# Kernel optimization log

Measured on AMD Instinct MI355X. Metric: run time of the kernel, lower is better.

Reference implementation:

```python
import jax, jax.numpy as jnp
import numpy as np

N = 16384      # tokens
D_IN = 256     # input feature dim
D = 1024       # d_model
H = 2048       # expert hidden dim (2 * d_model)
E = 8          # n_experts
K = 2          # top_k
OUT = 2        # output classes
EPS = 1e-5


def layernorm(x, g, b):
    m = jnp.mean(x, axis=-1, keepdims=True)
    v = jnp.mean(jnp.square(x - m), axis=-1, keepdims=True)
    return (x - m) * jax.lax.rsqrt(v + EPS) * g + b


def setup_inputs() -> dict:
    key = jax.random.key(0)
    ks = jax.random.split(key, 10)
    s_in = 1.0 / np.sqrt(D_IN)
    s_d = 1.0 / np.sqrt(D)
    s_h = 1.0 / np.sqrt(H)
    return {
        "x": jax.random.normal(ks[0], (N, D_IN), jnp.float32),
        "w_in": jax.random.normal(ks[1], (D_IN, D), jnp.float32) * s_in,
        "b_in": jnp.zeros((D,), jnp.float32),
        "g_in": jnp.ones((D,), jnp.float32),
        "beta_in": jnp.zeros((D,), jnp.float32),
        "w_gate": jax.random.normal(ks[2], (D, E), jnp.float32) * s_d,
        "w1": jax.random.normal(ks[3], (E, D, H), jnp.float32) * s_d,
        "b1": jnp.zeros((E, H), jnp.float32),
        "w2": jax.random.normal(ks[4], (E, H, D), jnp.float32) * s_h,
        "b2": jnp.zeros((E, D), jnp.float32),
        "g_moe": jnp.ones((D,), jnp.float32),
        "beta_moe": jnp.zeros((D,), jnp.float32),
        "g_out": jnp.ones((D,), jnp.float32),
        "beta_out": jnp.zeros((D,), jnp.float32),
        "w_cls": jax.random.normal(ks[5], (D, OUT), jnp.float32) * s_d,
        "b_cls": jnp.zeros((OUT,), jnp.float32),
    }


def reference(x, w_in, b_in, g_in, beta_in, w_gate, w1, b1, w2, b2,
              g_moe, beta_moe, g_out, beta_out, w_cls, b_cls):
    # input projection + norm
    h = layernorm(x @ w_in + b_in, g_in, beta_in)            # [N, D]
    # router: softmax then top-k, renormalize over selected experts
    probs = jax.nn.softmax(h @ w_gate, axis=-1)              # [N, E]
    _, top_idx = jax.lax.top_k(probs, K)                     # [N, K]
    sel = jax.nn.one_hot(top_idx, E, dtype=probs.dtype).sum(axis=1)  # [N, E] 0/1
    gates = probs * sel
    gates = gates / (jnp.sum(gates, axis=-1, keepdims=True) + 1e-9)
    # experts: weighted combine; gate==0 tokens contribute nothing (same math
    # as the torch masked gather/scatter-add, dropout off in eval)
    mixed = jnp.zeros_like(h)
    for e in range(E):  # fixed, small expert count
        expert_out = jax.nn.gelu(h @ w1[e] + b1[e]) @ w2[e] + b2[e]  # [N, D]
        mixed = mixed + gates[:, e:e + 1] * expert_out
    out = layernorm(h + mixed, g_moe, beta_moe)
    out = layernorm(out, g_out, beta_out)
    return out @ w_cls + b_cls                               # [N, OUT]
```

## Files before the change

kernel.cpp:

```cpp
#include <hip/hip_runtime.h>
#include <hip/hip_bf16.h>

#define D_IN 256
#define DM   1024
#define HD   2048
#define NE   8
#define NTOK 16384

typedef __attribute__((ext_vector_type(8))) short short8;
typedef __attribute__((ext_vector_type(4))) float f32x4;
typedef unsigned int uint;

#define MT_TOFF1 0
#define MT_TOFF2 512
#define MT_CNT1  1536
#define MT_P1    1600
#define MT_OFF1  1664
#define MT_CNT2  1728
#define MT_PCNT2 1856
#define MT_TOTAL 1984

__device__ inline ushort f2bf(float v){
  __hip_bfloat16 b = __float2bfloat16(v);
  return *reinterpret_cast<ushort*>(&b);
}
__device__ inline float bf2f(ushort u){
  __hip_bfloat16 b = *reinterpret_cast<__hip_bfloat16*>(&u);
  return __bfloat162float(b);
}

__device__ inline float gelu_fast(float x){
  float u = 0.7978845608028654f * x * (1.0f + 0.044715f*x*x);
  return x / (1.0f + __expf(-2.0f*u));
}

__device__ inline void gload16(const void* g, void* l){
  __builtin_amdgcn_global_load_lds(
      (const __attribute__((address_space(1))) void*)g,
      (__attribute__((address_space(3))) void*)l, 16, 0, 0);
}

__global__ __launch_bounds__(256) void transpose_bf16_kernel(
    const float* __restrict__ src, ushort* __restrict__ dst, int R, int C)
{
  __shared__ float tile[32][33];
  int e = blockIdx.z;
  src += (size_t)e*R*C; dst += (size_t)e*R*C;
  int c0 = blockIdx.x*32, r0 = blockIdx.y*32;
  int tx = threadIdx.x & 31, ty = threadIdx.x >> 5;
  #pragma unroll
  for (int rr = ty; rr < 32; rr += 8)
    tile[rr][tx] = src[(size_t)(r0+rr)*C + c0+tx];
  __syncthreads();
  #pragma unroll
  for (int rr = ty; rr < 32; rr += 8)
    dst[(size_t)(c0+rr)*R + r0+tx] = f2bf(tile[tx][rr]);
}

__global__ __launch_bounds__(64) void build_xs6(
    const float* __restrict__ x, ushort* __restrict__ xs6)
{
  int row = blockIdx.x; int t = threadIdx.x;
  const float* xr = x + (size_t)row*D_IN;
  ushort* o = xs6 + (size_t)row*1536;
  #pragma unroll
  for (int i=0;i<4;++i){
    int c = t*4+i;
    float f = xr[c];
    ushort h = f2bf(f);        float fh = bf2f(h);
    ushort m = f2bf(f - fh);   float fm = bf2f(m);
    ushort lo = f2bf(f - fh - fm);
    o[c]      = h;  o[512+c]  = h;  o[1280+c] = h;
    o[256+c]  = m;  o[768+c]  = m;
    o[1024+c] = lo;
  }
}

__global__ __launch_bounds__(256) void build_wt6(
    const float* __restrict__ src, ushort* __restrict__ dst)
{
  __shared__ float tile[32][33];
  int c0 = blockIdx.x*32, r0 = blockIdx.y*32;
  int tx = threadIdx.x & 31, ty = threadIdx.x >> 5;
  #pragma unroll
  for (int rr = ty; rr < 32; rr += 8)
    tile[rr][tx] = src[(size_t)(r0+rr)*DM + c0+tx];
  __syncthreads();
  #pragma unroll
  for (int rr = ty; rr < 32; rr += 8){
    float f = tile[tx][rr];
    ushort h = f2bf(f);        float fh = bf2f(h);
    ushort m = f2bf(f - fh);   float fm = bf2f(m);
    ushort lo = f2bf(f - fh - fm);
    ushort* d = dst + (size_t)(c0+rr)*1536 + r0 + tx;
    d[0]    = h;  d[256]  = h;  d[1024] = h;
    d[512]  = m;  d[768]  = m;
    d[1280] = lo;
  }
}

__global__ __launch_bounds__(256) void wgate_t_kernel(
    const float* __restrict__ w_gate, float* __restrict__ wgt)
{
  int e = blockIdx.x;
  for (int j = threadIdx.x; j < DM; j += 256)
    wgt[(size_t)e*DM + j] = w_gate[(size_t)j*NE + e];
}

template<int MODE>
__global__ __launch_bounds__(512, 2) void gemm8p(
    const ushort* __restrict__ A,
    const ushort* __restrict__ BT,
    const int*   __restrict__ rows,
    const uint*  __restrict__ pcnt,
    const uint*  __restrict__ off1,
    const float* __restrict__ bias,
    float* __restrict__ yout,
    ushort* __restrict__ t1,
    int N, int K, int CH)
{
  __shared__ ushort lds[2][2][2][8192];
  const int tid = threadIdx.x;
  const int wid = tid>>6, l = tid&63;
  const int wm = wid>>2, wn = wid&3;
  const int lr = l&15, lk = l>>4;

  int e = 0;
  const int bn0 = blockIdx.x*256;
  const int bm0 = blockIdx.y*256;
  if (MODE==1){
    e = blockIdx.z;
    if ((uint)bm0 >= pcnt[e]) return;
  }
  const ushort* Bbase = BT + (MODE==1 ? (size_t)e*N*K : (size_t)0);

  const ushort* aS[2][2]; const ushort* bS[2][2];
  #pragma unroll
  for (int h=0;h<2;++h){
    #pragma unroll
    for (int j=0;j<2;++j){
      int idx = j*512 + tid;
      int r   = idx>>3;
      int cb  = ((idx&7)*16) ^ (((r>>2)&1)<<5);
      if (MODE==1){
        int id = rows[e*CH + bm0 + h*128 + r];
        aS[h][j] = A + (size_t)id*K + (cb>>1);
      } else {
        aS[h][j] = A + (size_t)(bm0 + h*128 + r)*K + (cb>>1);
      }
      bS[h][j] = Bbase + (size_t)(bn0 + h*128 + r)*K + (cb>>1);
    }
  }

  auto stageA = [&](int db, int kt){
    #pragma unroll
    for (int h=0;h<2;++h)
      #pragma unroll
      for (int j=0;j<2;++j)
        gload16(aS[h][j] + kt, &lds[db][0][h][(j*512+tid)*8]);
  };
  auto stageB = [&](int db, int kt){
    #pragma unroll
    for (int h=0;h<2;++h)
      #pragma unroll
      for (int j=0;j<2;++j)
        gload16(bS[h][j] + kt, &lds[db][1][h][(j*512+tid)*8]);
  };

  stageA(0, 0);  stageB(0, 0);
  stageA(1, 64); stageB(1, 64);
  asm volatile("s_waitcnt vmcnt(8)" ::: "memory");
  __builtin_amdgcn_s_barrier();

  const char* aB; const char* bB;
  auto ldA = [&](int frA, int ks)->short8{
    int r = frA*16 + lr;
    int off = r*128 + ((ks*64 + lk*16) ^ (((r>>2)&1)<<5));
    return *(const short8*)(aB + off);
  };
  auto ldB = [&](int fc, int ks)->short8{
    int r = (wn&1)*64 + fc*16 + lr;
    int off = r*128 + ((ks*64 + lk*16) ^ (((r>>2)&1)<<5));
    return *(const short8*)(bB + off);
  };

  short8 aR[4][2]; short8 bR[4][2];
  f32x4 acc[8][4] = {};
  const int NT = K>>6;

  for (int T=0; T<NT; ++T){
    const int cur = T&1;
    aB = (const char*)&lds[cur][0][wm][0];
    bB = (const char*)&lds[cur][1][wn>>1][0];
    const bool pf = (T+2 < NT);
    const int kpf = (T+2)<<6;

    #pragma unroll
    for (int fr=0;fr<4;++fr){ aR[fr][0]=ldA(fr,0); aR[fr][1]=ldA(fr,1); }
    #pragma unroll
    for (int fc=0;fc<2;++fc){ bR[fc][0]=ldB(fc,0); bR[fc][1]=ldB(fc,1); }
    __builtin_amdgcn_s_barrier();
    __builtin_amdgcn_s_setprio(1);
    #pragma unroll
    for (int fr=0;fr<4;++fr)
      #pragma unroll
      for (int fc=0;fc<2;++fc)
        #pragma unroll
        for (int ks=0;ks<2;++ks)
          acc[fr][fc] = __builtin_amdgcn_mfma_f32_16x16x32_bf16(aR[fr][ks], bR[fc][ks], acc[fr][fc], 0,0,0);
    __builtin_amdgcn_s_setprio(0);
    __builtin_amdgcn_s_barrier();

    #pragma unroll
    for (int fc=0;fc<2;++fc){ bR[2+fc][0]=ldB(2+fc,0); bR[2+fc][1]=ldB(2+fc,1); }
    __builtin_amdgcn_s_barrier();
    __builtin_amdgcn_s_setprio(1);
    #pragma unroll
    for (int fr=0;fr<4;++fr)
      #pragma unroll
      for (int fc=0;fc<2;++fc)
        #pragma unroll
        for (int ks=0;ks<2;++ks)
          acc[fr][2+fc] = __builtin_amdgcn_mfma_f32_16x16x32_bf16(aR[fr][ks], bR[2+fc][ks], acc[fr][2+fc], 0,0,0);
    __builtin_amdgcn_s_setprio(0);
    __builtin_amdgcn_s_barrier();

    #pragma unroll
    for (int fr=0;fr<4;++fr){ aR[fr][0]=ldA(4+fr,0); aR[fr][1]=ldA(4+fr,1); }
    if (pf) stageB(cur, kpf);
    __builtin_amdgcn_s_barrier();
    __builtin_amdgcn_s_setprio(1);
    #pragma unroll
    for (int fr=0;fr<4;++fr)
      #pragma unroll
      for (int fc=0;fc<2;++fc)
        #pragma unroll
        for (int ks=0;ks<2;++ks)
          acc[4+fr][2+fc] = __builtin_amdgcn_mfma_f32_16x16x32_bf16(aR[fr][ks], bR[2+fc][ks], acc[4+fr][2+fc], 0,0,0);
    __builtin_amdgcn_s_setprio(0);
    __builtin_amdgcn_s_barrier();

    if (pf) stageA(cur, kpf);
    if (pf)              { asm volatile("s_waitcnt vmcnt(8)" ::: "memory"); }
    else if (T+1 < NT)   { asm volatile("s_waitcnt vmcnt(0)" ::: "memory"); }
    __builtin_amdgcn_s_barrier();
    __builtin_amdgcn_s_setprio(1);
    #pragma unroll
    for (int fr=0;fr<4;++fr)
      #pragma unroll
      for (int fc=0;fc<2;++fc)
        #pragma unroll
        for (int ks=0;ks<2;++ks)
          acc[4+fr][fc] = __builtin_amdgcn_mfma_f32_16x16x32_bf16(aR[fr][ks], bR[fc][ks], acc[4+fr][fc], 0,0,0);
    __builtin_amdgcn_s_setprio(0);
    __builtin_amdgcn_s_barrier();
  }

  const float* bp = bias + (MODE==1 ? (size_t)e*N : (size_t)0);
  #pragma unroll
  for (int fr=0;fr<8;++fr){
    #pragma unroll
    for (int fc=0;fc<4;++fc){
      int n = bn0 + wn*64 + fc*16 + lr;
      float bb = bp[n];
      #pragma unroll
      for (int v=0;v<4;++v){
        int mloc = wm*128 + fr*16 + lk*4 + v;
        float val = acc[fr][fc][v] + bb;
        if (MODE==0){
          yout[(size_t)(bm0+mloc)*N + n] = val;
        } else {
          t1[((size_t)off1[e] + bm0 + mloc)*N + n] = f2bf(gelu_fast(val));
        }
      }
    }
  }
}

__device__ inline double wredd(double v){
  #pragma unroll
  for (int o=32;o>0;o>>=1) v += __shfl_xor(v, o, 64);
  return v;
}

__global__ __launch_bounds__(256) void ln_router_kernel(
    const float* __restrict__ g_in, const float* __restrict__ beta_in,
    const float* __restrict__ wgt,
    ushort* __restrict__ hbf, float* __restrict__ resid,
    float* __restrict__ gates, int* __restrict__ selmask)
{
  int tok = blockIdx.x*4 + (threadIdx.x>>6);
  int l = threadIdx.x & 63;
  float* row = resid + (size_t)tok*DM;
  float u[16];
  double s=0.0, q=0.0;
  #pragma unroll
  for (int r=0;r<16;++r){ u[r]=row[l+64*r]; s+=u[r]; q+=(double)u[r]*u[r]; }
  s = wredd(s); q = wredd(q);
  double mean = s*(1.0/1024.0);
  double var  = q*(1.0/1024.0) - mean*mean;
  double rstd = 1.0/sqrt(var + 1e-5);

  double lg[NE];
  #pragma unroll
  for (int e=0;e<NE;++e) lg[e]=0.0;
  float hv[16];
  #pragma unroll
  for (int r=0;r<16;++r){
    int j = l + 64*r;
    double v = ((double)u[r]-mean)*rstd*(double)g_in[j] + (double)beta_in[j];
    hv[r] = (float)v;
    #pragma unroll
    for (int e=0;e<NE;++e) lg[e] += v*(double)wgt[(size_t)e*DM + j];
  }
  #pragma unroll
  for (int r=0;r<16;++r){
    int j = l + 64*r;
    row[j] = hv[r];
    hbf[(size_t)tok*DM + j] = f2bf(hv[r]);
  }
  #pragma unroll
  for (int e=0;e<NE;++e) lg[e] = wredd(lg[e]);

  if (l==0){
    double mx = lg[0];
    #pragma unroll
    for (int e=1;e<NE;++e) mx = lg[e]>mx ? lg[e] : mx;
    double p[NE]; double sum=0.0;
    #pragma unroll
    for (int e=0;e<NE;++e){ p[e]=exp(lg[e]-mx); sum+=p[e]; }
    #pragma unroll
    for (int e=0;e<NE;++e) p[e]/=sum;
    int i1=0;
    for (int e=1;e<NE;++e) if (p[e]>p[i1]) i1=e;
    int i2=-1;
    for (int e=0;e<NE;++e){ if (e==i1) continue; if (i2<0 || p[e]>p[i2]) i2=e; }
    double denom = p[i1]+p[i2]+1e-9;
    float g[NE];
    #pragma unroll
    for (int e=0;e<NE;++e) g[e]=0.f;
    g[i1]=(float)(p[i1]/denom);
    g[i2]=(float)(p[i2]/denom);
    #pragma unroll
    for (int e=0;e<NE;++e) gates[(size_t)tok*NE+e]=g[e];
    selmask[tok] = (1<<i1)|(1<<i2);
  }
}

__global__ __launch_bounds__(256) void builder_count(
    const int* __restrict__ selmask, uint* __restrict__ bc1, uint* __restrict__ bc2)
{
  __shared__ uint c1[8], c2s[16];
  int b = blockIdx.x, tid = threadIdx.x;
  if (tid<8) c1[tid]=0;
  if (tid<16) c2s[tid]=0;
  __syncthreads();
  int m = selmask[b*256+tid];
  int ea = __ffs(m)-1, eb = 31-__clz(m);
  atomicAdd(&c1[ea],1u); atomicAdd(&c1[eb],1u);
  atomicAdd(&c2s[ea],1u); atomicAdd(&c2s[8+eb],1u);
  __syncthreads();
  if (tid<8) bc1[b*8+tid]=c1[tid];
  if (tid<16) bc2[b*16+tid]=c2s[tid];
}

__global__ __launch_bounds__(256) void builder_scan(
    const uint* __restrict__ bc1, const uint* __restrict__ bc2,
    uint* __restrict__ meta, int nch, int TPC)
{
  int tid = threadIdx.x;
  int c = tid/24, k = tid%24;
  if (c < nch){
    if (k < 8){
      uint run=0;
      for (int b=c*TPC; b<(c+1)*TPC; ++b){ meta[MT_TOFF1 + b*8 + k] = run; run += bc1[b*8+k]; }
      meta[MT_CNT1 + c*8 + k] = run;
    } else {
      int k2 = k-8;
      uint run=0;
      for (int b=c*TPC; b<(c+1)*TPC; ++b){ meta[MT_TOFF2 + b*16 + k2] = run; run += bc2[b*16+k2]; }
      meta[MT_CNT2 + c*16 + k2] = run;
      meta[MT_PCNT2 + c*16 + k2] = ((run + 127u)/128u)*128u;
    }
  }
  __syncthreads();
  if (tid < nch){
    uint off=0;
    for (int e=0;e<8;++e){
      uint cn = meta[MT_CNT1 + tid*8 + e];
      uint p = ((cn+255u)/256u)*256u;
      meta[MT_P1 + tid*8 + e] = p;
      meta[MT_OFF1 + tid*8 + e] = off;
      off += p;
    }
  }
}

__device__ inline int exclscan256(int v, int* sc, int tid){
  sc[tid]=v; __syncthreads();
  #pragma unroll
  for (int o=1;o<256;o<<=1){
    int x = (tid>=o) ? sc[tid-o] : 0;
    __syncthreads();
    sc[tid]+=x;
    __syncthreads();
  }
  int incl = sc[tid]; __syncthreads();
  return incl - v;
}

__global__ __launch_bounds__(256) void builder_fill(
    const int* __restrict__ selmask, const uint* __restrict__ meta,
    int* __restrict__ ids1, int* __restrict__ g2row, int* __restrict__ g2tok,
    int CH)
{
  __shared__ int sc[256];
  int b = blockIdx.x, tid = threadIdx.x;
  int t = b*256 + tid;
  int c = t / CH;
  int m = selmask[t];
  int ea = __ffs(m)-1, eb = 31-__clz(m);
  int ja=0, jb=0;
  for (int e=0;e<8;++e){
    int r0 = exclscan256((ea==e)?1:0, sc, tid);
    if (ea==e) ja = r0;
    int r1 = exclscan256((eb==e)?1:0, sc, tid);
    if (eb==e) jb = r1;
  }
  {
    uint j    = meta[MT_TOFF2 + b*16 + ea] + (uint)ja;
    uint pos1 = j;
    uint row  = meta[MT_OFF1 + c*8 + ea] + pos1;
    ids1[(c*8+ea)*CH + pos1] = t;
    g2row[((c*2+0)*8+ea)*CH + j] = (int)row;
    g2tok[((c*2+0)*8+ea)*CH + j] = t;
  }
  {
    uint j    = meta[MT_TOFF2 + b*16 + 8 + eb] + (uint)jb;
    uint pos1 = meta[MT_CNT2 + c*16 + eb] + j;
    uint row  = meta[MT_OFF1 + c*8 + eb] + pos1;
    ids1[(c*8+eb)*CH + pos1] = t;
    g2row[((c*2+1)*8+eb)*CH + j] = (int)row;
    g2tok[((c*2+1)*8+eb)*CH + j] = t;
  }
}

template<int EPI>
__global__ __launch_bounds__(256) void gemm_sparse(
    const ushort* __restrict__ Abase,
    const ushort* __restrict__ BT,
    const int*   __restrict__ rows,
    const int*   __restrict__ toks,
    const uint*  __restrict__ pcnt,
    const uint*  __restrict__ cnt,
    const uint*  __restrict__ off1,
    const float* __restrict__ bias,
    const float* __restrict__ gates,
    ushort* __restrict__ t1,
    float*  __restrict__ resid,
    int K, int N, int CH)
{
  const int e = blockIdx.z;
  const int bm0 = blockIdx.y*128;
  if ((uint)bm0 >= pcnt[e]) return;
  const int bn0 = blockIdx.x*128;

  __shared__ ushort As[128*32];
  __shared__ ushort Bs[128*32];
  const int tid = threadIdx.x;
  const int w = tid>>6, l = tid&63;
  const int wm = w>>1, wn = w&1;
  const int lr = l&15, lk = l>>4;
  const int rsub = l>>2, csub = (l&3)*8;

  const ushort* ag[2]; const ushort* bg[2];
  ushort* al[2]; ushort* bl[2];
  #pragma unroll
  for (int i=0;i<2;++i){
    int ra = w*32 + i*16 + rsub;
    int id = rows[e*CH + bm0 + ra];
    ag[i] = Abase + (size_t)id*K + csub;
    int rb = bn0 + w*32 + i*16 + rsub;
    bg[i] = BT + (size_t)e*N*K + (size_t)rb*K + csub;
    al[i] = (ushort*)As + (w*32 + i*16)*32;
    bl[i] = (ushort*)Bs + (w*32 + i*16)*32;
  }

  f32x4 zero = {0.f,0.f,0.f,0.f};
  f32x4 acc[4][4];
  #pragma unroll
  for (int i=0;i<4;++i){
    #pragma unroll
    for (int j=0;j<4;++j) acc[i][j]=zero;
  }

  for (int kt = 0; kt < K; kt += 32) {
    #pragma unroll
    for (int i=0;i<2;++i){
      gload16(ag[i]+kt, al[i]);
      gload16(bg[i]+kt, bl[i]);
    }
    __syncthreads();
    short8 af[4], bf[4];
    #pragma unroll
    for (int i=0;i<4;++i) af[i] = *(const short8*)(As + (wm*64 + i*16 + lr)*32 + lk*8);
    #pragma unroll
    for (int j=0;j<4;++j) bf[j] = *(const short8*)(Bs + (wn*64 + j*16 + lr)*32 + lk*8);
    #pragma unroll
    for (int i=0;i<4;++i){
      #pragma unroll
      for (int j=0;j<4;++j)
        acc[i][j] = __builtin_amdgcn_mfma_f32_16x16x32_bf16(af[i], bf[j], acc[i][j], 0, 0, 0);
    }
    __syncthreads();
  }

  #pragma unroll
  for (int i=0;i<4;++i){
    #pragma unroll
    for (int j=0;j<4;++j){
      int n = bn0 + wn*64 + j*16 + lr;
      float bn_ = bias[(size_t)e*N + n];
      #pragma unroll
      for (int r=0;r<4;++r){
        int mloc = wm*64 + i*16 + lk*4 + r;
        float v = acc[i][j][r] + bn_;
        if (EPI==0){
          size_t trow = (size_t)off1[e] + bm0 + mloc;
          t1[trow*N + n] = f2bf(gelu_fast(v));
        } else {
          int mg = bm0 + mloc;
          if ((uint)mg < cnt[e]){
            int tok = toks[e*CH + mg];
            float g = gates[(size_t)tok*NE + e];
            resid[(size_t)tok*N + n] += g*v;
          }
        }
      }
    }
  }
}

__global__ __launch_bounds__(64) void final_kernel(
    const float* __restrict__ resid,
    const float* __restrict__ g_moe, const float* __restrict__ beta_moe,
    const float* __restrict__ g_out, const float* __restrict__ beta_out,
    const float* __restrict__ w_cls, const float* __restrict__ b_cls,
    float* __restrict__ out)
{
  int tok = blockIdx.x; int l = threadIdx.x;
  const float* row = resid + (size_t)tok*DM;
  float u[16];
  double s=0.0,q=0.0;
  #pragma unroll
  for (int r=0;r<16;++r){ u[r]=row[l + 64*r]; s+=u[r]; q+=(double)u[r]*u[r]; }
  s=wredd(s); q=wredd(q);
  double m1 = s*(1.0/1024.0), v1 = q*(1.0/1024.0)-m1*m1;
  double rs1 = 1.0/sqrt(v1+1e-5);
  float tv[16]; double s2=0.0,q2=0.0;
  #pragma unroll
  for (int r=0;r<16;++r){
    int j = l+64*r;
    float vv = (float)((u[r]-m1)*rs1)*g_moe[j] + beta_moe[j];
    tv[r]=vv; s2+=vv; q2+=(double)vv*vv;
  }
  s2=wredd(s2); q2=wredd(q2);
  double m2=s2*(1.0/1024.0), v2=q2*(1.0/1024.0)-m2*m2;
  double rs2=1.0/sqrt(v2+1e-5);
  double p0=0.0,p1=0.0;
  #pragma unroll
  for (int r=0;r<16;++r){
    int j=l+64*r;
    double y=((double)tv[r]-m2)*rs2*(double)g_out[j]+(double)beta_out[j];
    p0+=y*(double)w_cls[j*2]; p1+=y*(double)w_cls[j*2+1];
  }
  p0=wredd(p0); p1=wredd(p1);
  if (l==0){
    out[(size_t)tok*2  ]=(float)(p0+(double)b_cls[0]);
    out[(size_t)tok*2+1]=(float)(p1+(double)b_cls[1]);
  }
}

extern "C" void kernel_launch(void* const* d_in, const int* in_sizes, int n_in,
                              void* d_out, int out_size, void* d_ws, size_t ws_size,
                              hipStream_t stream)
{
  (void)in_sizes; (void)n_in; (void)out_size;
  const float* x       = (const float*)d_in[0];
  const float* w_in    = (const float*)d_in[1];
  const float* b_in    = (const float*)d_in[2];
  const float* g_in    = (const float*)d_in[3];
  const float* beta_in = (const float*)d_in[4];
  const float* w_gate  = (const float*)d_in[5];
  const float* w1      = (const float*)d_in[6];
  const float* b1      = (const float*)d_in[7];
  const float* w2      = (const float*)d_in[8];
  const float* b2      = (const float*)d_in[9];
  const float* g_moe   = (const float*)d_in[10];
  const float* beta_mo = (const float*)d_in[11];
  const float* g_out   = (const float*)d_in[12];
  const float* beta_ou = (const float*)d_in[13];
  const float* w_cls   = (const float*)d_in[14];
  const float* b_cls   = (const float*)d_in[15];
  float* out = (float*)d_out;

  char* p = (char*)d_ws;
  ushort* w1t   = (ushort*)p; p += (size_t)NE*HD*DM*2;
  ushort* w2t   = (ushort*)p; p += (size_t)NE*DM*HD*2;
  ushort* hbf   = (ushort*)p; p += (size_t)NTOK*DM*2;
  float*  resid = (float*)p;  p += (size_t)NTOK*DM*4;
  float*  gates = (float*)p;  p += (size_t)NTOK*NE*4;
  int*    selmk = (int*)p;    p += (size_t)NTOK*4;
  int*    ids1  = (int*)p;    p += (size_t)NE*NTOK*4;
  int*    g2row = (int*)p;    p += (size_t)2*NE*NTOK*4;
  int*    g2tok = (int*)p;    p += (size_t)2*NE*NTOK*4;
  float*  wgt   = (float*)p;  p += (size_t)NE*DM*4;
  uint*   bc1   = (uint*)p;   p += (size_t)64*8*4;
  uint*   bc2   = (uint*)p;   p += (size_t)64*16*4;
  uint*   meta  = (uint*)p;   p += (size_t)MT_TOTAL*4;
  size_t fixed = (size_t)(p - (char*)d_ws);

  const size_t xs6_bytes = (size_t)NTOK*1536*2;
  const size_t wt6_bytes = (size_t)DM*1536*2;
  const size_t router_bytes = xs6_bytes + wt6_bytes;
  size_t t1b2 = ((size_t)2*(NTOK/2)+2048)*HD*2;
  size_t t1b4 = ((size_t)2*(NTOK/4)+2048)*HD*2;
  int nch = 8;
  if (ws_size >= fixed + (t1b2 > router_bytes ? t1b2 : router_bytes)) nch = 2;
  else if (ws_size >= fixed + (t1b4 > router_bytes ? t1b4 : router_bytes)) nch = 4;
  const int CH  = NTOK/nch;
  const int TPC = CH/256;
  ushort* t1  = (ushort*)p;
  ushort* xs6 = (ushort*)p;
  ushort* wt6 = (ushort*)(p + xs6_bytes);

  build_xs6<<<dim3(NTOK), 64, 0, stream>>>(x, xs6);
  build_wt6<<<dim3(DM/32, D_IN/32), 256, 0, stream>>>(w_in, wt6);
  wgate_t_kernel<<<dim3(NE), 256, 0, stream>>>(w_gate, wgt);
  transpose_bf16_kernel<<<dim3(HD/32, DM/32, NE), 256, 0, stream>>>(w1, w1t, DM, HD);
  transpose_bf16_kernel<<<dim3(DM/32, HD/32, NE), 256, 0, stream>>>(w2, w2t, HD, DM);

  gemm8p<0><<<dim3(DM/256, NTOK/256), 512, 0, stream>>>(
      xs6, wt6, nullptr, nullptr, nullptr, b_in, resid, nullptr, DM, 1536, CH);
  ln_router_kernel<<<dim3(NTOK/4), 256, 0, stream>>>(g_in, beta_in, wgt,
                                                     hbf, resid, gates, selmk);

  hipMemsetAsync(ids1, 0, (size_t)NE*NTOK*4, stream);
  hipMemsetAsync(g2row, 0, (size_t)2*NE*NTOK*4, stream);
  hipMemsetAsync(g2tok, 0, (size_t)2*NE*NTOK*4, stream);

  builder_count<<<dim3(NTOK/256), 256, 0, stream>>>(selmk, bc1, bc2);
  builder_scan<<<dim3(1), 256, 0, stream>>>(bc1, bc2, meta, nch, TPC);
  builder_fill<<<dim3(NTOK/256), 256, 0, stream>>>(selmk, meta, ids1, g2row, g2tok, CH);

  for (int c = 0; c < nch; ++c) {
    gemm8p<1><<<dim3(HD/256, CH/256, NE), 512, 0, stream>>>(
        hbf, w1t, ids1 + (size_t)c*8*CH,
        meta+MT_P1+c*8, meta+MT_OFF1+c*8,
        b1, nullptr, t1, HD, DM, CH);
    for (int s = 0; s < 2; ++s) {
      gemm_sparse<1><<<dim3(DM/128, CH/128, NE), 256, 0, stream>>>(
          t1, w2t, g2row + (size_t)(c*2+s)*8*CH, g2tok + (size_t)(c*2+s)*8*CH,
          meta+MT_PCNT2+c*16+s*8, meta+MT_CNT2+c*16+s*8, nullptr,
          b2, gates, nullptr, resid, HD, DM, CH);
    }
  }

  final_kernel<<<dim3(NTOK), 64, 0, stream>>>(resid, g_moe, beta_mo, g_out, beta_ou,
                                              w_cls, b_cls, out);
}
```

Measured before the change: 926.3 us.

## Route second expert GEMM through pipelined 256x256 gemm8p kernel with full XOR swizzle

```diff
diff --git a/kernel.cpp b/kernel.cpp
--- a/kernel.cpp
+++ b/kernel.cpp
@@ -112,11 +112,15 @@
     const ushort* __restrict__ A,
     const ushort* __restrict__ BT,
     const int*   __restrict__ rows,
+    const int*   __restrict__ toks,
     const uint*  __restrict__ pcnt,
+    const uint*  __restrict__ cnt,
     const uint*  __restrict__ off1,
     const float* __restrict__ bias,
+    const float* __restrict__ gates,
     float* __restrict__ yout,
     ushort* __restrict__ t1,
+    float*  __restrict__ resid,
     int N, int K, int CH)
 {
   __shared__ ushort lds[2][2][2][8192];
@@ -128,11 +132,11 @@
   int e = 0;
   const int bn0 = blockIdx.x*256;
   const int bm0 = blockIdx.y*256;
-  if (MODE==1){
+  if (MODE>=1){
     e = blockIdx.z;
     if ((uint)bm0 >= pcnt[e]) return;
   }
-  const ushort* Bbase = BT + (MODE==1 ? (size_t)e*N*K : (size_t)0);
+  const ushort* Bbase = BT + (MODE>=1 ? (size_t)e*N*K : (size_t)0);
 
   const ushort* aS[2][2]; const ushort* bS[2][2];
   #pragma unroll
@@ -141,14 +145,14 @@
     for (int j=0;j<2;++j){
       int idx = j*512 + tid;
       int r   = idx>>3;
-      int cb  = ((idx&7)*16) ^ (((r>>2)&1)<<5);
-      if (MODE==1){
+      int cu  = ((idx&7) ^ (r&7)) * 8;
+      if (MODE>=1){
         int id = rows[e*CH + bm0 + h*128 + r];
-        aS[h][j] = A + (size_t)id*K + (cb>>1);
+        aS[h][j] = A + (size_t)id*K + cu;
       } else {
-        aS[h][j] = A + (size_t)(bm0 + h*128 + r)*K + (cb>>1);
+        aS[h][j] = A + (size_t)(bm0 + h*128 + r)*K + cu;
       }
-      bS[h][j] = Bbase + (size_t)(bn0 + h*128 + r)*K + (cb>>1);
+      bS[h][j] = Bbase + (size_t)(bn0 + h*128 + r)*K + cu;
     }
   }
 
@@ -175,12 +179,12 @@
   const char* aB; const char* bB;
   auto ldA = [&](int frA, int ks)->short8{
     int r = frA*16 + lr;
-    int off = r*128 + ((ks*64 + lk*16) ^ (((r>>2)&1)<<5));
+    int off = r*128 + (((ks*4 + lk) ^ (r&7))<<4);
     return *(const short8*)(aB + off);
   };
   auto ldB = [&](int fc, int ks)->short8{
     int r = (wn&1)*64 + fc*16 + lr;
-    int off = r*128 + ((ks*64 + lk*16) ^ (((r>>2)&1)<<5));
+    int off = r*128 + (((ks*4 + lk) ^ (r&7))<<4);
     return *(const short8*)(bB + off);
   };
 
@@ -256,7 +260,7 @@
     __builtin_amdgcn_s_barrier();
   }
 
-  const float* bp = bias + (MODE==1 ? (size_t)e*N : (size_t)0);
+  const float* bp = bias + (MODE>=1 ? (size_t)e*N : (size_t)0);
   #pragma unroll
   for (int fr=0;fr<8;++fr){
     #pragma unroll
@@ -269,8 +273,15 @@
         float val = acc[fr][fc][v] + bb;
         if (MODE==0){
           yout[(size_t)(bm0+mloc)*N + n] = val;
+        } else if (MODE==1){
+          t1[((size_t)off1[e] + bm0 + mloc)*N + n] = f2bf(gelu_fast(val));
         } else {
-          t1[((size_t)off1[e] + bm0 + mloc)*N + n] = f2bf(gelu_fast(val));
+          int mg = bm0 + mloc;
+          if ((uint)mg < cnt[e]){
+            int tok = toks[e*CH + mg];
+            float g = gates[(size_t)tok*NE + e];
+            resid[(size_t)tok*N + n] += g*val;
+          }
         }
       }
     }
@@ -380,7 +391,7 @@
       uint run=0;
       for (int b=c*TPC; b<(c+1)*TPC; ++b){ meta[MT_TOFF2 + b*16 + k2] = run; run += bc2[b*16+k2]; }
       meta[MT_CNT2 + c*16 + k2] = run;
-      meta[MT_PCNT2 + c*16 + k2] = ((run + 127u)/128u)*128u;
+      meta[MT_PCNT2 + c*16 + k2] = ((run + 255u)/256u)*256u;
     }
   }
   __syncthreads();
@@ -442,102 +453,6 @@
     ids1[(c*8+eb)*CH + pos1] = t;
     g2row[((c*2+1)*8+eb)*CH + j] = (int)row;
     g2tok[((c*2+1)*8+eb)*CH + j] = t;
-  }
-}
-
-template<int EPI>
-__global__ __launch_bounds__(256) void gemm_sparse(
-    const ushort* __restrict__ Abase,
-    const ushort* __restrict__ BT,
-    const int*   __restrict__ rows,
-    const int*   __restrict__ toks,
-    const uint*  __restrict__ pcnt,
-    const uint*  __restrict__ cnt,
-    const uint*  __restrict__ off1,
-    const float* __restrict__ bias,
-    const float* __restrict__ gates,
-    ushort* __restrict__ t1,
-    float*  __restrict__ resid,
-    int K, int N, int CH)
-{
-  const int e = blockIdx.z;
-  const int bm0 = blockIdx.y*128;
-  if ((uint)bm0 >= pcnt[e]) return;
-  const int bn0 = blockIdx.x*128;
-
-  __shared__ ushort As[128*32];
-  __shared__ ushort Bs[128*32];
-  const int tid = threadIdx.x;
-  const int w = tid>>6, l = tid&63;
-  const int wm = w>>1, wn = w&1;
-  const int lr = l&15, lk = l>>4;
-  const int rsub = l>>2, csub = (l&3)*8;
-
-  const ushort* ag[2]; const ushort* bg[2];
-  ushort* al[2]; ushort* bl[2];
-  #pragma unroll
-  for (int i=0;i<2;++i){
-    int ra = w*32 + i*16 + rsub;
-    int id = rows[e*CH + bm0 + ra];
-    ag[i] = Abase + (size_t)id*K + csub;
-    int rb = bn0 + w*32 + i*16 + rsub;
-    bg[i] = BT + (size_t)e*N*K + (size_t)rb*K + csub;
-    al[i] = (ushort*)As + (w*32 + i*16)*32;
-    bl[i] = (ushort*)Bs + (w*32 + i*16)*32;
-  }
-
-  f32x4 zero = {0.f,0.f,0.f,0.f};
-  f32x4 acc[4][4];
-  #pragma unroll
-  for (int i=0;i<4;++i){
-    #pragma unroll
-    for (int j=0;j<4;++j) acc[i][j]=zero;
-  }
-
-  for (int kt = 0; kt < K; kt += 32) {
-    #pragma unroll
-    for (int i=0;i<2;++i){
-      gload16(ag[i]+kt, al[i]);
-      gload16(bg[i]+kt, bl[i]);
-    }
-    __syncthreads();
-    short8 af[4], bf[4];
-    #pragma unroll
-    for (int i=0;i<4;++i) af[i] = *(const short8*)(As + (wm*64 + i*16 + lr)*32 + lk*8);
-    #pragma unroll
-    for (int j=0;j<4;++j) bf[j] = *(const short8*)(Bs + (wn*64 + j*16 + lr)*32 + lk*8);
-    #pragma unroll
-    for (int i=0;i<4;++i){
-      #pragma unroll
-      for (int j=0;j<4;++j)
-        acc[i][j] = __builtin_amdgcn_mfma_f32_16x16x32_bf16(af[i], bf[j], acc[i][j], 0, 0, 0);
-    }
-    __syncthreads();
-  }
-
-  #pragma unroll
-  for (int i=0;i<4;++i){
-    #pragma unroll
-    for (int j=0;j<4;++j){
-      int n = bn0 + wn*64 + j*16 + lr;
-      float bn_ = bias[(size_t)e*N + n];
-      #pragma unroll
-      for (int r=0;r<4;++r){
-        int mloc = wm*64 + i*16 + lk*4 + r;
-        float v = acc[i][j][r] + bn_;
-        if (EPI==0){
-          size_t trow = (size_t)off1[e] + bm0 + mloc;
-          t1[trow*N + n] = f2bf(gelu_fast(v));
-        } else {
-          int mg = bm0 + mloc;
-          if ((uint)mg < cnt[e]){
-            int tok = toks[e*CH + mg];
-            float g = gates[(size_t)tok*NE + e];
-            resid[(size_t)tok*N + n] += g*v;
-          }
-        }
-      }
-    }
   }
 }
 
@@ -641,7 +556,8 @@
   transpose_bf16_kernel<<<dim3(DM/32, HD/32, NE), 256, 0, stream>>>(w2, w2t, HD, DM);
 
   gemm8p<0><<<dim3(DM/256, NTOK/256), 512, 0, stream>>>(
-      xs6, wt6, nullptr, nullptr, nullptr, b_in, resid, nullptr, DM, 1536, CH);
+      xs6, wt6, nullptr, nullptr, nullptr, nullptr, nullptr, b_in, nullptr,
+      resid, nullptr, nullptr, DM, 1536, CH);
   ln_router_kernel<<<dim3(NTOK/4), 256, 0, stream>>>(g_in, beta_in, wgt,
                                                      hbf, resid, gates, selmk);
 
@@ -655,14 +571,14 @@
 
   for (int c = 0; c < nch; ++c) {
     gemm8p<1><<<dim3(HD/256, CH/256, NE), 512, 0, stream>>>(
-        hbf, w1t, ids1 + (size_t)c*8*CH,
-        meta+MT_P1+c*8, meta+MT_OFF1+c*8,
-        b1, nullptr, t1, HD, DM, CH);
+        hbf, w1t, ids1 + (size_t)c*8*CH, nullptr,
+        meta+MT_P1+c*8, nullptr, meta+MT_OFF1+c*8,
+        b1, nullptr, nullptr, t1, nullptr, HD, DM, CH);
     for (int s = 0; s < 2; ++s) {
-      gemm_sparse<1><<<dim3(DM/128, CH/128, NE), 256, 0, stream>>>(
+      gemm8p<2><<<dim3(DM/256, CH/256, NE), 512, 0, stream>>>(
           t1, w2t, g2row + (size_t)(c*2+s)*8*CH, g2tok + (size_t)(c*2+s)*8*CH,
           meta+MT_PCNT2+c*16+s*8, meta+MT_CNT2+c*16+s*8, nullptr,
-          b2, gates, nullptr, resid, HD, DM, CH);
+          b2, gates, nullptr, nullptr, resid, DM, HD, CH);
     }
   }
 
```

After: 1.025 ms. 1.11x slower.
